# Performance work log

Hardware: AMD Instinct MI355X
Metric: run time of the kernel (lower is better)

Reference implementation:

```python
import jax, jax.numpy as jnp
import numpy as np
import math

EMB = 512
HEADS = 8
FM = 56
WS = 7


def _relative_position_index(ws):
    coords = np.stack(np.meshgrid(np.arange(ws), np.arange(ws), indexing='ij')).reshape(2, -1)
    rel = coords[:, :, None] - coords[:, None, :]            # [2, ws^2, ws^2]
    rel = rel.transpose(1, 2, 0)                              # [ws^2, ws^2, 2]
    rel = rel + np.abs(rel.min())                             # shift to >= 0 (adds ws-1)
    rel[:, :, 0] = rel[:, :, 0] * (2 * ws - 1)
    return rel.sum(-1)                                        # [ws^2, ws^2] int

REL_IDX = jnp.asarray(_relative_position_index(WS))


def setup_inputs() -> dict:
    key = jax.random.key(0)
    ks = jax.random.split(key, 8)
    B, L, E = 16, FM * FM, EMB
    scale = 0.02
    return {
        'x': jax.random.normal(ks[0], (B, L, E), dtype=jnp.float32),
        'q_w': jax.random.normal(ks[1], (E, E), dtype=jnp.float32) * scale,
        'q_b': jax.random.normal(ks[2], (E,), dtype=jnp.float32) * scale,
        'k_w': jax.random.normal(ks[3], (E, E), dtype=jnp.float32) * scale,
        'k_b': jax.random.normal(ks[4], (E,), dtype=jnp.float32) * scale,
        'v_w': jax.random.normal(ks[5], (E, E), dtype=jnp.float32) * scale,
        'v_b': jax.random.normal(ks[6], (E,), dtype=jnp.float32) * scale,
        'bias_table': jax.random.normal(ks[7], ((2 * WS - 1) ** 2, HEADS), dtype=jnp.float32) * scale,
    }


def reference(x, q_w, q_b, k_w, k_b, v_w, v_b, bias_table):
    B, L, E = x.shape
    nh, d, ws = HEADS, E // HEADS, WS
    n = ws * ws
    # Faithful to the torch code: reshape (NOT channels-last transpose), then window partition
    xr = x.reshape(B, E, FM, FM)
    w = xr.reshape(B, FM // ws, ws, FM // ws, ws, E)
    w = jnp.transpose(w, (0, 1, 3, 2, 4, 5)).reshape(B, -1, ws, ws, E)  # [B, nW, ws, ws, E]
    nW = w.shape[1]
    # Linear projections (torch Linear: x @ W.T + b)
    q = (w @ q_w.T + q_b).reshape(B, nW, nh, n, d)
    k = (w @ k_w.T + k_b).reshape(B, nW, nh, n, d)
    v = (w @ v_w.T + v_b).reshape(B, nW, nh, n, d)
    # Relative position bias: [nh, n, n]
    bias = bias_table[REL_IDX.reshape(-1)].reshape(n, n, nh).transpose(2, 0, 1)
    scores = jnp.einsum('bwhqd,bwhkd->bwhqk', q, k) / math.sqrt(d)
    scores = scores + bias[None, None]
    attn = jax.nn.softmax(scores, axis=-1)
    out = jnp.einsum('bwhqk,bwhkd->bwhqd', attn, v)
    return out.reshape(B, L, E)
```

## Files before the change

### kernel.cpp

```cpp
#include <hip/hip_runtime.h>

typedef __attribute__((ext_vector_type(8))) short short8;
typedef __attribute__((ext_vector_type(4))) short short4v;
typedef __attribute__((ext_vector_type(4))) float float4v;
typedef __attribute__((ext_vector_type(8))) __bf16 bf16x8;

#define LDS_PQ 57344
#define LDS_PK 107520
#define LDS_BIAS 157696
#define LDS_TOTAL 163104

__device__ __forceinline__ unsigned short f2bf(float f) {
  unsigned u = __float_as_uint(f);
  u += 0x7FFFu + ((u >> 16) & 1u);
  return (unsigned short)(u >> 16);
}

__device__ __forceinline__ int pswz(int s) { return ((s ^ (s >> 3)) & 7) << 4; }

__global__ void wconv_kernel(const float* __restrict__ qw, const float* __restrict__ kw,
                             const float* __restrict__ vw, short* __restrict__ out) {
  int idx = blockIdx.x * 256 + threadIdx.x;
  int g = idx >> 15;
  int rem = idx & 32767;
  int lane = rem & 63;
  int n01 = (rem >> 6) & 1;
  int w   = (rem >> 7) & 15;
  int kk  = rem >> 11;
  int o  = w * 32 + n01 * 16 + (lane & 15);
  int k0 = kk * 32 + (lane >> 4) * 8;
  const float* src = (g == 0) ? qw : (g == 1) ? kw : vw;
  const float* p = src + o * 512 + k0;
  float4v v0 = *(const float4v*)(p);
  float4v v1 = *(const float4v*)(p + 4);
  short8 o8;
  o8[0] = (short)f2bf(v0.x); o8[1] = (short)f2bf(v0.y);
  o8[2] = (short)f2bf(v0.z); o8[3] = (short)f2bf(v0.w);
  o8[4] = (short)f2bf(v1.x); o8[5] = (short)f2bf(v1.y);
  o8[6] = (short)f2bf(v1.z); o8[7] = (short)f2bf(v1.w);
  *(short8*)(out + idx * 8) = o8;
}

__global__ __launch_bounds__(1024, 4) void wattn_kernel(
    const float* __restrict__ x, const short* __restrict__ wcvt,
    const float* __restrict__ qb, const float* __restrict__ kb, const float* __restrict__ vb,
    const float* __restrict__ btab, float* __restrict__ out) {
  __shared__ __align__(16) char sm[LDS_TOTAL];
  const int tid  = threadIdx.x;
  const int lane = tid & 63;
  const int wave = tid >> 6;
  const int bwi  = blockIdx.x;
  const int bb   = bwi >> 6, wi = bwi & 63;
  const int l15  = lane & 15;
  const int l4   = lane >> 4;
  const int ig   = l4 * 4;

  for (int i = tid; i < 169 * 8; i += 1024)
    *(float*)(sm + LDS_BIAS + i * 4) = btab[i];

  {
    const float* xb = x + (size_t)bb * (3136 * 512);
    const int whi = (wi >> 3) * 7, wlo = (wi & 7) * 7;
    for (int idx = tid; idx < 49 * 128; idx += 1024) {
      int t = idx >> 7, c4 = idx & 127;
      int yt = (t * 37) >> 8, xt = t - yt * 7;
      int l = (whi + yt) * 56 + wlo + xt;
      float4v v = *(const float4v*)(xb + l * 512 + c4 * 4);
      short4v o;
      o.x = (short)f2bf(v.x); o.y = (short)f2bf(v.y);
      o.z = (short)f2bf(v.z); o.w = (short)f2bf(v.w);
      int byte = t * 1024 + c4 * 8;
      *(short4v*)(sm + (byte ^ ((t & 7) << 4))) = o;
    }
  }
  __syncthreads();

  const int wcol = wave * 32;

  int xbase[4], xsw[4];
#pragma unroll
  for (int mt = 0; mt < 4; ++mt) {
    int row = mt * 16 + l15;
    xbase[mt] = row * 1024;
    xsw[mt]   = (row & 7) << 4;
  }

  const short* wgb0 = wcvt + wave * 1024 + lane * 8;

  for (int g = 0; g < 3; ++g) {
    const short* wgb = wgb0 + g * 262144;
    const float* bias = (g == 0) ? qb : (g == 1) ? kb : vb;
    float4v acc[2][4];
#pragma unroll
    for (int nt = 0; nt < 2; ++nt)
#pragma unroll
      for (int mt = 0; mt < 4; ++mt) acc[nt][mt] = (float4v)0.f;

    bf16x8 w0 = __builtin_bit_cast(bf16x8, *(const short8*)(wgb));
    bf16x8 w1 = __builtin_bit_cast(bf16x8, *(const short8*)(wgb + 512));

#pragma unroll 1
    for (int kk = 0; kk < 16; ++kk) {
      const int nko = ((kk + 1) & 15) * 16384;
      bf16x8 nw0 = __builtin_bit_cast(bf16x8, *(const short8*)(wgb + nko));
      bf16x8 nw1 = __builtin_bit_cast(bf16x8, *(const short8*)(wgb + nko + 512));
      const int c = kk * 64 + l4 * 16;
      bf16x8 xf[4];
#pragma unroll
      for (int mt = 0; mt < 4; ++mt)
        xf[mt] = __builtin_bit_cast(bf16x8, *(const short8*)(sm + xbase[mt] + (c ^ xsw[mt])));
#pragma unroll
      for (int mt = 0; mt < 4; ++mt) {
        acc[0][mt] = __builtin_amdgcn_mfma_f32_16x16x32_bf16(w0, xf[mt], acc[0][mt], 0, 0, 0);
        acc[1][mt] = __builtin_amdgcn_mfma_f32_16x16x32_bf16(w1, xf[mt], acc[1][mt], 0, 0, 0);
      }
      w0 = nw0;
      w1 = nw1;
    }

    if (g < 2) {
      const int base = (g == 0) ? LDS_PQ : LDS_PK;
#pragma unroll
      for (int nt = 0; nt < 2; ++nt) {
        int o0 = wcol + nt * 16 + ig;
        float4v bv = *(const float4v*)(bias + o0);
        int dd0 = o0 & 63, sg = o0 >> 6;
#pragma unroll
        for (int mt = 0; mt < 4; ++mt) {
          int t = mt * 16 + l15;
          if (t < 49) {
            int s = t * 8 + sg;
            short4v pk;
#pragma unroll
            for (int r = 0; r < 4; ++r) pk[r] = (short)f2bf(acc[nt][mt][r] + bv[r]);
            *(short4v*)(sm + base + ((s * 128 + dd0 * 2) ^ pswz(s))) = pk;
          }
        }
      }
    } else {
      __syncthreads();
#pragma unroll
      for (int nt = 0; nt < 2; ++nt) {
        int o0 = wcol + nt * 16 + ig;
        float4v bv = *(const float4v*)(bias + o0);
        int dd0 = o0 & 63, sg = o0 >> 6;
#pragma unroll
        for (int mt = 0; mt < 4; ++mt) {
          int t = mt * 16 + l15;
          if (t < 49) {
            int s = t * 8 + sg;
            int h2 = (s * 1339) >> 16;
            int tp = s - h2 * 49;
            char* p = sm + h2 * 7168 + tp * 2;
#pragma unroll
            for (int r = 0; r < 4; ++r)
              *(unsigned short*)(p + (dd0 + r) * 112) = f2bf(acc[nt][mt][r] + bv[r]);
          }
        }
      }
      if (tid < 512) {
        int h2 = tid >> 6, dd = tid & 63;
        char* p = sm + h2 * 7168 + dd * 112;
#pragma unroll
        for (int q = 49; q < 56; ++q) *(unsigned short*)(p + q * 2) = 0;
      }
      __syncthreads();
    }
  }

  const int h  = wave & 7;
  const int mh = wave >> 3;
  const float* bias_f = (const float*)(sm + LDS_BIAS);

  float4v sc[4][2];
#pragma unroll
  for (int jt = 0; jt < 4; ++jt)
#pragma unroll
    for (int it = 0; it < 2; ++it) sc[jt][it] = (float4v)0.f;

#pragma unroll
  for (int ks = 0; ks < 2; ++ks) {
    const int dd = ks * 32 + l4 * 8;
    bf16x8 kf[4], qf[2];
#pragma unroll
    for (int jt = 0; jt < 4; ++jt) {
      int s = h * 49 + jt * 16 + l15;
      int flat = s * 128 + dd * 2;
      kf[jt] = __builtin_bit_cast(bf16x8, *(const short8*)(sm + LDS_PK + (flat ^ pswz(s))));
    }
#pragma unroll
    for (int it = 0; it < 2; ++it) {
      int s = h * 49 + (mh * 2 + it) * 16 + l15;
      int flat = s * 128 + dd * 2;
      qf[it] = __builtin_bit_cast(bf16x8, *(const short8*)(sm + LDS_PQ + (flat ^ pswz(s))));
    }
#pragma unroll
    for (int jt = 0; jt < 4; ++jt)
#pragma unroll
      for (int it = 0; it < 2; ++it)
        sc[jt][it] = __builtin_amdgcn_mfma_f32_16x16x32_bf16(kf[jt], qf[it], sc[jt][it], 0, 0, 0);
  }

#pragma unroll
  for (int it = 0; it < 2; ++it) {
    int i = (mh * 2 + it) * 16 + l15;
    int yi = (i * 37) >> 8, xi = i - yi * 7;
    float mx = -1e30f;
#pragma unroll
    for (int jt = 0; jt < 4; ++jt)
#pragma unroll
      for (int r = 0; r < 4; ++r) {
        int j = jt * 16 + ig + r;
        float v = -1e30f;
        if (i < 49 && j < 49) {
          int yj = (j * 37) >> 8, xj = j - yj * 7;
          int idx = (yi - yj + 6) * 13 + (xi - xj + 6);
          v = sc[jt][it][r] * 0.125f + bias_f[idx * 8 + h];
        }
        sc[jt][it][r] = v;
        mx = fmaxf(mx, v);
      }
    mx = fmaxf(mx, __shfl_xor(mx, 16));
    mx = fmaxf(mx, __shfl_xor(mx, 32));
    float ssum = 0.f;
#pragma unroll
    for (int jt = 0; jt < 4; ++jt)
#pragma unroll
      for (int r = 0; r < 4; ++r) {
        float e = __expf(sc[jt][it][r] - mx);
        sc[jt][it][r] = e;
        ssum += e;
      }
    ssum += __shfl_xor(ssum, 16);
    ssum += __shfl_xor(ssum, 32);
    float inv = 1.f / ssum;
#pragma unroll
    for (int jt = 0; jt < 4; ++jt)
#pragma unroll
      for (int r = 0; r < 4; ++r) sc[jt][it][r] *= inv;
  }

  __syncthreads();
  const int ovb = LDS_PQ + h * 8192;
#pragma unroll
  for (int it = 0; it < 2; ++it) {
    int i = (mh * 2 + it) * 16 + l15;
    if (i < 49) {
      int rowb = i * 128;
      int swz = (i & 7) << 4;
#pragma unroll
      for (int jt = 0; jt < 4; ++jt) {
        short4v pk;
#pragma unroll
        for (int r = 0; r < 4; ++r) pk[r] = (short)f2bf(sc[jt][it][r]);
        *(short4v*)(sm + ovb + ((rowb + jt * 32 + ig * 2) ^ swz)) = pk;
      }
    }
  }
  __syncthreads();

  float4v oacc[4][2];
#pragma unroll
  for (int dt = 0; dt < 4; ++dt)
#pragma unroll
    for (int tt = 0; tt < 2; ++tt) oacc[dt][tt] = (float4v)0.f;

#pragma unroll
  for (int ks = 0; ks < 2; ++ks) {
    const int tp0 = ks * 32 + l4 * 8;
    const int tc  = (tp0 >= 56) ? 0 : tp0;
    bf16x8 vf[4], af[2];
#pragma unroll
    for (int dt = 0; dt < 4; ++dt) {
      int dd = dt * 16 + l15;
      vf[dt] = __builtin_bit_cast(bf16x8, *(const short8*)(sm + h * 7168 + dd * 112 + tc * 2));
    }
#pragma unroll
    for (int tt = 0; tt < 2; ++tt) {
      int t = (mh * 2 + tt) * 16 + l15;
      int flat = t * 128 + tp0 * 2;
      af[tt] = __builtin_bit_cast(bf16x8, *(const short8*)(sm + ovb + (flat ^ ((t & 7) << 4))));
    }
#pragma unroll
    for (int dt = 0; dt < 4; ++dt)
#pragma unroll
      for (int tt = 0; tt < 2; ++tt)
        oacc[dt][tt] = __builtin_amdgcn_mfma_f32_16x16x32_bf16(vf[dt], af[tt], oacc[dt][tt], 0, 0, 0);
  }

  float* op = out + (size_t)bwi * 25088 + h * 3136;
#pragma unroll
  for (int tt = 0; tt < 2; ++tt) {
    int t = (mh * 2 + tt) * 16 + l15;
    if (t < 49) {
#pragma unroll
      for (int dt = 0; dt < 4; ++dt)
        *(float4v*)(op + t * 64 + dt * 16 + ig) = oacc[dt][tt];
    }
  }
}

extern "C" void kernel_launch(void* const* d_in, const int* in_sizes, int n_in,
                              void* d_out, int out_size, void* d_ws, size_t ws_size,
                              hipStream_t stream) {
  const float* x    = (const float*)d_in[0];
  const float* q_w  = (const float*)d_in[1];
  const float* q_b  = (const float*)d_in[2];
  const float* k_w  = (const float*)d_in[3];
  const float* k_b  = (const float*)d_in[4];
  const float* v_w  = (const float*)d_in[5];
  const float* v_b  = (const float*)d_in[6];
  const float* btab = (const float*)d_in[7];
  short* wcvt = (short*)d_ws;

  hipLaunchKernelGGL(wconv_kernel, dim3(384), dim3(256), 0, stream, q_w, k_w, v_w, wcvt);
  hipLaunchKernelGGL(wattn_kernel, dim3(1024), dim3(1024), 0, stream,
                     x, wcvt, q_b, k_b, v_b, btab, (float*)d_out);
}
```

Before: 165.1 us.

## Deepen weight prefetch, fold softmax scale into Q, swizzle V layout, drop barriers

```diff
diff --git a/kernel.cpp b/kernel.cpp
--- a/kernel.cpp
+++ b/kernel.cpp
@@ -76,6 +76,7 @@
   __syncthreads();
 
   const int wcol = wave * 32;
+  const int ck   = l4 * 16;
 
   int xbase[4], xsw[4];
 #pragma unroll
@@ -87,6 +88,24 @@
 
   const short* wgb0 = wcvt + wave * 1024 + lane * 8;
 
+#define LDW(OFF) __builtin_bit_cast(bf16x8, *(const short8*)(wgb + (OFF)))
+#define GEMM_PHASE(KIDX, W0, W1)                                                          \
+  do {                                                                                    \
+    const int c_ = (KIDX) * 64 + ck;                                                      \
+    bf16x8 x0_ = __builtin_bit_cast(bf16x8, *(const short8*)(sm + xbase[0] + (c_ ^ xsw[0]))); \
+    bf16x8 x1_ = __builtin_bit_cast(bf16x8, *(const short8*)(sm + xbase[1] + (c_ ^ xsw[1]))); \
+    bf16x8 x2_ = __builtin_bit_cast(bf16x8, *(const short8*)(sm + xbase[2] + (c_ ^ xsw[2]))); \
+    bf16x8 x3_ = __builtin_bit_cast(bf16x8, *(const short8*)(sm + xbase[3] + (c_ ^ xsw[3]))); \
+    acc[0][0] = __builtin_amdgcn_mfma_f32_16x16x32_bf16(W0, x0_, acc[0][0], 0, 0, 0);     \
+    acc[1][0] = __builtin_amdgcn_mfma_f32_16x16x32_bf16(W1, x0_, acc[1][0], 0, 0, 0);     \
+    acc[0][1] = __builtin_amdgcn_mfma_f32_16x16x32_bf16(W0, x1_, acc[0][1], 0, 0, 0);     \
+    acc[1][1] = __builtin_amdgcn_mfma_f32_16x16x32_bf16(W1, x1_, acc[1][1], 0, 0, 0);     \
+    acc[0][2] = __builtin_amdgcn_mfma_f32_16x16x32_bf16(W0, x2_, acc[0][2], 0, 0, 0);     \
+    acc[1][2] = __builtin_amdgcn_mfma_f32_16x16x32_bf16(W1, x2_, acc[1][2], 0, 0, 0);     \
+    acc[0][3] = __builtin_amdgcn_mfma_f32_16x16x32_bf16(W0, x3_, acc[0][3], 0, 0, 0);     \
+    acc[1][3] = __builtin_amdgcn_mfma_f32_16x16x32_bf16(W1, x3_, acc[1][3], 0, 0, 0);     \
+  } while (0)
+
   for (int g = 0; g < 3; ++g) {
     const short* wgb = wgb0 + g * 262144;
     const float* bias = (g == 0) ? qb : (g == 1) ? kb : vb;
@@ -96,30 +115,25 @@
 #pragma unroll
       for (int mt = 0; mt < 4; ++mt) acc[nt][mt] = (float4v)0.f;
 
-    bf16x8 w0 = __builtin_bit_cast(bf16x8, *(const short8*)(wgb));
-    bf16x8 w1 = __builtin_bit_cast(bf16x8, *(const short8*)(wgb + 512));
+    bf16x8 wa0 = LDW(0),         wa1 = LDW(512);
+    bf16x8 wb0 = LDW(16384),     wb1 = LDW(16384 + 512);
+    bf16x8 wc0, wc1, wd0, wd1;
 
 #pragma unroll 1
-    for (int kk = 0; kk < 16; ++kk) {
-      const int nko = ((kk + 1) & 15) * 16384;
-      bf16x8 nw0 = __builtin_bit_cast(bf16x8, *(const short8*)(wgb + nko));
-      bf16x8 nw1 = __builtin_bit_cast(bf16x8, *(const short8*)(wgb + nko + 512));
-      const int c = kk * 64 + l4 * 16;
-      bf16x8 xf[4];
-#pragma unroll
-      for (int mt = 0; mt < 4; ++mt)
-        xf[mt] = __builtin_bit_cast(bf16x8, *(const short8*)(sm + xbase[mt] + (c ^ xsw[mt])));
-#pragma unroll
-      for (int mt = 0; mt < 4; ++mt) {
-        acc[0][mt] = __builtin_amdgcn_mfma_f32_16x16x32_bf16(w0, xf[mt], acc[0][mt], 0, 0, 0);
-        acc[1][mt] = __builtin_amdgcn_mfma_f32_16x16x32_bf16(w1, xf[mt], acc[1][mt], 0, 0, 0);
-      }
-      w0 = nw0;
-      w1 = nw1;
+    for (int kk = 0; kk < 16; kk += 4) {
+      wc0 = LDW(((kk + 2) & 15) * 16384); wc1 = LDW(((kk + 2) & 15) * 16384 + 512);
+      GEMM_PHASE(kk, wa0, wa1);
+      wd0 = LDW(((kk + 3) & 15) * 16384); wd1 = LDW(((kk + 3) & 15) * 16384 + 512);
+      GEMM_PHASE(kk + 1, wb0, wb1);
+      wa0 = LDW(((kk + 4) & 15) * 16384); wa1 = LDW(((kk + 4) & 15) * 16384 + 512);
+      GEMM_PHASE(kk + 2, wc0, wc1);
+      wb0 = LDW(((kk + 5) & 15) * 16384); wb1 = LDW(((kk + 5) & 15) * 16384 + 512);
+      GEMM_PHASE(kk + 3, wd0, wd1);
     }
 
     if (g < 2) {
       const int base = (g == 0) ? LDS_PQ : LDS_PK;
+      const float qs = (g == 0) ? 0.125f : 1.0f;
 #pragma unroll
       for (int nt = 0; nt < 2; ++nt) {
         int o0 = wcol + nt * 16 + ig;
@@ -132,7 +146,7 @@
             int s = t * 8 + sg;
             short4v pk;
 #pragma unroll
-            for (int r = 0; r < 4; ++r) pk[r] = (short)f2bf(acc[nt][mt][r] + bv[r]);
+            for (int r = 0; r < 4; ++r) pk[r] = (short)f2bf((acc[nt][mt][r] + bv[r]) * qs);
             *(short4v*)(sm + base + ((s * 128 + dd0 * 2) ^ pswz(s))) = pk;
           }
         }
@@ -150,21 +164,24 @@
           if (t < 49) {
             int s = t * 8 + sg;
             int h2 = (s * 1339) >> 16;
-            int tp = s - h2 * 49;
-            char* p = sm + h2 * 7168 + tp * 2;
-#pragma unroll
-            for (int r = 0; r < 4; ++r)
-              *(unsigned short*)(p + (dd0 + r) * 112) = f2bf(acc[nt][mt][r] + bv[r]);
+            int colb = h2 * 112 + (s - h2 * 49) * 2;
+#pragma unroll
+            for (int r = 0; r < 4; ++r) {
+              int dd = dd0 + r;
+              *(unsigned short*)(sm + ((dd * 896 + colb) ^ ((dd & 7) << 4))) =
+                  f2bf(acc[nt][mt][r] + bv[r]);
+            }
           }
         }
       }
       if (tid < 512) {
         int h2 = tid >> 6, dd = tid & 63;
-        char* p = sm + h2 * 7168 + dd * 112;
-#pragma unroll
-        for (int q = 49; q < 56; ++q) *(unsigned short*)(p + q * 2) = 0;
-      }
-      __syncthreads();
+        int rowb = dd * 896 + h2 * 112;
+        int swz = (dd & 7) << 4;
+#pragma unroll
+        for (int q = 49; q < 56; ++q)
+          *(unsigned short*)(sm + ((rowb + q * 2) ^ swz)) = 0;
+      }
     }
   }
 
@@ -215,7 +232,7 @@
         if (i < 49 && j < 49) {
           int yj = (j * 37) >> 8, xj = j - yj * 7;
           int idx = (yi - yj + 6) * 13 + (xi - xj + 6);
-          v = sc[jt][it][r] * 0.125f + bias_f[idx * 8 + h];
+          v = sc[jt][it][r] + bias_f[idx * 8 + h];
         }
         sc[jt][it][r] = v;
         mx = fmaxf(mx, v);
@@ -240,23 +257,23 @@
       for (int r = 0; r < 4; ++r) sc[jt][it][r] *= inv;
   }
 
-  __syncthreads();
-  const int ovb = LDS_PQ + h * 8192;
 #pragma unroll
   for (int it = 0; it < 2; ++it) {
     int i = (mh * 2 + it) * 16 + l15;
     if (i < 49) {
-      int rowb = i * 128;
-      int swz = (i & 7) << 4;
+      int s = h * 49 + i;
+      int rowb = s * 128;
+      int swz = pswz(s);
 #pragma unroll
       for (int jt = 0; jt < 4; ++jt) {
         short4v pk;
 #pragma unroll
         for (int r = 0; r < 4; ++r) pk[r] = (short)f2bf(sc[jt][it][r]);
-        *(short4v*)(sm + ovb + ((rowb + jt * 32 + ig * 2) ^ swz)) = pk;
-      }
-    }
-  }
+        *(short4v*)(sm + LDS_PQ + ((rowb + jt * 32 + ig * 2) ^ swz)) = pk;
+      }
+    }
+  }
+
   __syncthreads();
 
   float4v oacc[4][2];
@@ -268,18 +285,20 @@
 #pragma unroll
   for (int ks = 0; ks < 2; ++ks) {
     const int tp0 = ks * 32 + l4 * 8;
-    const int tc  = (tp0 >= 56) ? 0 : tp0;
     bf16x8 vf[4], af[2];
 #pragma unroll
     for (int dt = 0; dt < 4; ++dt) {
       int dd = dt * 16 + l15;
-      vf[dt] = __builtin_bit_cast(bf16x8, *(const short8*)(sm + h * 7168 + dd * 112 + tc * 2));
+      vf[dt] = __builtin_bit_cast(bf16x8,
+          *(const short8*)(sm + ((dd * 896 + h * 112 + tp0 * 2) ^ ((dd & 7) << 4))));
     }
 #pragma unroll
     for (int tt = 0; tt < 2; ++tt) {
       int t = (mh * 2 + tt) * 16 + l15;
-      int flat = t * 128 + tp0 * 2;
-      af[tt] = __builtin_bit_cast(bf16x8, *(const short8*)(sm + ovb + (flat ^ ((t & 7) << 4))));
+      int tr = (t > 48) ? 48 : t;
+      int s = h * 49 + tr;
+      af[tt] = __builtin_bit_cast(bf16x8,
+          *(const short8*)(sm + LDS_PQ + ((s * 128 + tp0 * 2) ^ pswz(s))));
     }
 #pragma unroll
     for (int dt = 0; dt < 4; ++dt)
@@ -298,6 +317,8 @@
         *(float4v*)(op + t * 64 + dt * 16 + ig) = oacc[dt][tt];
     }
   }
+#undef LDW
+#undef GEMM_PHASE
 }
 
 extern "C" void kernel_launch(void* const* d_in, const int* in_sizes, int n_in,
```

After: 165.1 us. About the same (-0.0%).
